# Performance work log

Measured on AMD Instinct MI355X. Metric: run time of the kernel, lower is better.

## Reference

```python
import jax, jax.numpy as jnp
import numpy as np
import math

V, E, L, MLP_RATIO = 16384, 768, 5, 4
B, S = 4, 1024
EPS = 1e-5


def setup_inputs() -> dict:
    key = jax.random.key(0)
    ks = jax.random.split(key, 20)
    sd = 0.02
    H = E * MLP_RATIO
    inp = {}
    inp["seq"] = jax.random.randint(ks[0], (B, S), 0, V)
    inp["pad_mask"] = jnp.zeros((B, S), dtype=bool)
    inp["embed"] = jax.random.normal(ks[1], (V, E), jnp.float32) * sd
    inp["enc_qkv_w"] = jax.random.normal(ks[2], (L, 3, E, E), jnp.float32) * sd
    inp["enc_qkv_b"] = jnp.zeros((L, 3, E), jnp.float32)
    inp["enc_ln"] = jnp.stack([jnp.ones((L, 2, E)), jnp.zeros((L, 2, E))], axis=2)  # [L,2,2,E] (gamma,beta)
    inp["enc_mlp_w1"] = jax.random.normal(ks[3], (L, E, H), jnp.float32) * sd
    inp["enc_mlp_b1"] = jnp.zeros((L, H), jnp.float32)
    inp["enc_mlp_w2"] = jax.random.normal(ks[4], (L, H, E), jnp.float32) * sd
    inp["enc_mlp_b2"] = jnp.zeros((L, E), jnp.float32)
    inp["dec_qkv_w"] = jax.random.normal(ks[5], (L, 6, E, E), jnp.float32) * sd  # q,k,v,q2,k2,v2
    inp["dec_qkv_b"] = jnp.zeros((L, 6, E), jnp.float32)
    inp["dec_ln"] = jnp.stack([jnp.ones((L, 3, E)), jnp.zeros((L, 3, E))], axis=2)  # [L,3,2,E]
    inp["dec_mlp_w1"] = jax.random.normal(ks[6], (L, E, H), jnp.float32) * sd
    inp["dec_mlp_b1"] = jnp.zeros((L, H), jnp.float32)
    inp["dec_mlp_w2"] = jax.random.normal(ks[7], (L, H, E), jnp.float32) * sd
    inp["dec_mlp_b2"] = jnp.zeros((L, E), jnp.float32)
    inp["unembed"] = jax.random.normal(ks[8], (E, V), jnp.float32) * sd
    return inp


def _layernorm(x, g, b):
    mu = jnp.mean(x, axis=-1, keepdims=True)
    var = jnp.mean((x - mu) ** 2, axis=-1, keepdims=True)
    return (x - mu) * jax.lax.rsqrt(var + EPS) * g + b


def reference(seq, pad_mask, embed, enc_qkv_w, enc_qkv_b, enc_ln,
              enc_mlp_w1, enc_mlp_b1, enc_mlp_w2, enc_mlp_b2,
              dec_qkv_w, dec_qkv_b, dec_ln,
              dec_mlp_w1, dec_mlp_b1, dec_mlp_w2, dec_mlp_b2, unembed):
    Bv, Sv = seq.shape
    Ev = embed.shape[1]
    scalar = 1.0 / math.sqrt(Ev)

    # RoPE tables over full E (single-head, as in source)
    inv_freq = 1.0 / (10000.0 ** (jnp.arange(0, Ev, 2, dtype=jnp.float32) / Ev))
    pos = jnp.arange(Sv, dtype=jnp.float32)
    freqs = pos[:, None] * inv_freq[None, :]  # [S, E/2]
    cos, sin = jnp.cos(freqs), jnp.sin(freqs)

    def rope(x):  # x: [B,S,E]
        x1, x2 = x[..., 0::2], x[..., 1::2]
        return jnp.stack((x1 * cos - x2 * sin, x1 * sin + x2 * cos), axis=-1).reshape(x.shape)

    neg = jnp.finfo(embed.dtype).min
    pad = pad_mask[:, None, :]  # [B,1,S] mask keys
    causal = jnp.triu(jnp.ones((Sv, Sv), dtype=bool), k=1)[None]  # [1,S,S]

    def attend(q, k, v, mask):
        scores = jnp.einsum('bse,bte->bst', q, k) * scalar
        scores = jnp.where(mask, neg, scores)
        return jnp.einsum('bst,bte->bse', jax.nn.softmax(scores, axis=-1), v)

    embeds = embed[seq]  # [B,S,E]

    # ---- encoder ----
    x = embeds
    enc_outs = []
    for i in range(enc_qkv_w.shape[0]):
        q = rope(x @ enc_qkv_w[i, 0] + enc_qkv_b[i, 0])
        k = rope(x @ enc_qkv_w[i, 1] + enc_qkv_b[i, 1])
        v = x @ enc_qkv_w[i, 2] + enc_qkv_b[i, 2]
        h = attend(q, k, v, pad)
        x = _layernorm(x + h, enc_ln[i, 0, 0], enc_ln[i, 0, 1])
        mlp = jax.nn.relu(jax.nn.relu(x @ enc_mlp_w1[i] + enc_mlp_b1[i]) @ enc_mlp_w2[i] + enc_mlp_b2[i])
        x = _layernorm(x + mlp, enc_ln[i, 1, 0], enc_ln[i, 1, 1])
        enc_outs.append(x)

    # ---- decoder ----
    x = embeds
    self_mask = causal | pad  # [B,S,S]
    for i in range(dec_qkv_w.shape[0]):
        kv = enc_outs[i]
        q = rope(x @ dec_qkv_w[i, 0] + dec_qkv_b[i, 0])
        k = rope(x @ dec_qkv_w[i, 1] + dec_qkv_b[i, 1])
        v = x @ dec_qkv_w[i, 2] + dec_qkv_b[i, 2]
        h1 = attend(q, k, v, self_mask)
        x = _layernorm(x + h1, dec_ln[i, 0, 0], dec_ln[i, 0, 1])
        q2 = rope(x @ dec_qkv_w[i, 3] + dec_qkv_b[i, 3])
        k2 = rope(kv @ dec_qkv_w[i, 4] + dec_qkv_b[i, 4])
        v2 = kv @ dec_qkv_w[i, 5] + dec_qkv_b[i, 5]
        h2 = attend(q2, k2, v2, pad)
        x = _layernorm(x + h2, dec_ln[i, 1, 0], dec_ln[i, 1, 1])
        mlp = jax.nn.relu(jax.nn.relu(x @ dec_mlp_w1[i] + dec_mlp_b1[i]) @ dec_mlp_w2[i] + dec_mlp_b2[i])
        x = _layernorm(x + mlp, dec_ln[i, 2, 0], dec_ln[i, 2, 1])

    return x @ unembed  # [B,S,V] logits
```

## Files before the change

### kernel.cpp

```cpp
#include <hip/hip_runtime.h>
#include <math.h>
#include <stdint.h>

#define B_ 4
#define S_ 1024
#define E_ 768
#define H_ 3072
#define V_ 16384
#define L_ 5
#define T_TOK 4096

typedef unsigned short u16;
typedef short bf16x8 __attribute__((ext_vector_type(8)));
typedef float floatx4 __attribute__((ext_vector_type(4)));
typedef u16 u16x4 __attribute__((ext_vector_type(4)));

__device__ __forceinline__ u16 f2bf(float f) {
    union { float f; unsigned u; } x; x.f = f;
    unsigned r = (x.u + 0x7FFFu + ((x.u >> 16) & 1u)) >> 16;
    return (u16)r;
}
__device__ __forceinline__ float bf2f(u16 v) {
    union { unsigned u; float f; } x; x.u = ((unsigned)v) << 16;
    return x.f;
}

__device__ __forceinline__ void gload16(const void* g, void* l) {
    __builtin_amdgcn_global_load_lds(
        (const __attribute__((address_space(1))) unsigned int*)(uintptr_t)g,
        (__attribute__((address_space(3))) unsigned int*)(uintptr_t)l,
        16, 0, 0);
}

__device__ __forceinline__ void bar_sync() {
    asm volatile("s_waitcnt vmcnt(0)" ::: "memory");
    __builtin_amdgcn_s_barrier();
    asm volatile("" ::: "memory");
}

__device__ __forceinline__ float rope_rot(float v, long row, long col, int lane,
                                          const float2* __restrict__ tab) {
    float vp = __shfl_xor(v, 1, 64);
    int s = (int)(row & (S_ - 1));
    int ii = ((int)col >> 1) % 384;
    float2 f = tab[(long)s * 384 + ii];
    return (lane & 1) ? (vp * f.y + v * f.x) : (v * f.x - vp * f.y);
}

#define BK 32

template<int OBF, int RELU, int BIAS, int ROPE>
__global__ __launch_bounds__(256) void mgemm(
    const u16* __restrict__ A, const u16* __restrict__ B, void* __restrict__ Cv,
    const float* __restrict__ bias, const float2* __restrict__ tab,
    float alpha, int M, int N, int K,
    int lda, int ldb, int ldc,
    long sA, long sB, long sC)
{
    __shared__ u16 As[2][128 * BK];
    __shared__ u16 Bs[2][128 * BK];

    const int tid  = threadIdx.x;
    const int lane = tid & 63;
    const int wid  = tid >> 6;
    const int wr   = (wid >> 1) * 64;
    const int wc   = (wid & 1) * 64;
    const int lr   = lane & 15;
    const int kg   = lane >> 4;

    const long rowBase = (long)blockIdx.y * 128;
    const long colBase = (long)blockIdx.x * 128;

    const u16* Ab = A + (long)blockIdx.z * sA;
    const u16* Bb = B + (long)blockIdx.z * sB;

    const int c0 = tid, c1 = tid + 256;
    const int ar0 = c0 >> 2, ac0 = (c0 & 3) ^ ((ar0 >> 1) & 3);
    const int ar1 = c1 >> 2, ac1 = (c1 & 3) ^ ((ar1 >> 1) & 3);

    const u16* pa0 = Ab + (rowBase + ar0) * (long)lda + ac0 * 8;
    const u16* pa1 = Ab + (rowBase + ar1) * (long)lda + ac1 * 8;
    const u16* pb0 = Bb + (colBase + ar0) * (long)ldb + ac0 * 8;
    const u16* pb1 = Bb + (colBase + ar1) * (long)ldb + ac1 * 8;

    int aoff[4], boff[4];
    #pragma unroll
    for (int m = 0; m < 4; ++m) {
        int r = wr + m * 16 + lr;
        aoff[m] = r * 32 + ((kg ^ ((r >> 1) & 3)) << 3);
        int c = wc + m * 16 + lr;
        boff[m] = c * 32 + ((kg ^ ((c >> 1) & 3)) << 3);
    }

    floatx4 acc[4][4];
    #pragma unroll
    for (int m = 0; m < 4; ++m)
        #pragma unroll
        for (int n = 0; n < 4; ++n)
            acc[m][n] = (floatx4)0.f;

    auto stage = [&](int buf, int k0) {
        gload16(pa0 + k0, &As[buf][c0 * 8]);
        gload16(pa1 + k0, &As[buf][c1 * 8]);
        gload16(pb0 + k0, &Bs[buf][c0 * 8]);
        gload16(pb1 + k0, &Bs[buf][c1 * 8]);
    };

    const int NT = K / BK;
    stage(0, 0);
    bar_sync();

    for (int t = 0; t < NT; ++t) {
        const int cur = t & 1;
        if (t + 1 < NT) stage(cur ^ 1, (t + 1) * BK);

        bf16x8 af[4], bfr[4];
        #pragma unroll
        for (int m = 0; m < 4; ++m) af[m]  = *(const bf16x8*)(&As[cur][aoff[m]]);
        #pragma unroll
        for (int n = 0; n < 4; ++n) bfr[n] = *(const bf16x8*)(&Bs[cur][boff[n]]);
        #pragma unroll
        for (int m = 0; m < 4; ++m)
            #pragma unroll
            for (int n = 0; n < 4; ++n)
                acc[m][n] = __builtin_amdgcn_mfma_f32_16x16x32_bf16(
                                af[m], bfr[n], acc[m][n], 0, 0, 0);

        if (t + 1 < NT) bar_sync();
    }

    const long col0 = colBase + wc + lr;
    const long row0 = rowBase + wr + kg * 4;
    #pragma unroll
    for (int n = 0; n < 4; ++n) {
        long col = col0 + n * 16;
        float bvc = (BIAS == 1) ? bias[col] : 0.f;
        #pragma unroll
        for (int m = 0; m < 4; ++m)
            #pragma unroll
            for (int j = 0; j < 4; ++j) {
                long row = row0 + m * 16 + j;
                float v = acc[m][n][j] * alpha + bvc;
                if (BIAS == 2) v += bias[row];
                if (ROPE) v = rope_rot(v, row, col, lane, tab);
                if (RELU) v = fmaxf(v, 0.f);
                if (OBF) ((u16*)Cv + (long)blockIdx.z * sC)[row * (long)ldc + col] = f2bf(v);
                else     ((float*)Cv + (long)blockIdx.z * sC)[row * (long)ldc + col] = v;
            }
    }
}

template<int OBF, int RELU, int BIAS, int ROPE>
__global__ __launch_bounds__(256) void mgemm64(
    const u16* __restrict__ A, const u16* __restrict__ B, void* __restrict__ Cv,
    const float* __restrict__ bias, const float2* __restrict__ tab,
    float alpha, int M, int N, int K,
    int lda, int ldb, int ldc,
    long sA, long sB, long sC)
{
    __shared__ u16 As[2][64 * BK];
    __shared__ u16 Bs[2][128 * BK];

    const int tid  = threadIdx.x;
    const int lane = tid & 63;
    const int wid  = tid >> 6;
    const int lr   = lane & 15;
    const int kg   = lane >> 4;

    const long rowBase = (long)blockIdx.y * 64;
    const long colBase = (long)blockIdx.x * 128;

    const u16* Ab = A + (long)blockIdx.z * sA;
    const u16* Bb = B + (long)blockIdx.z * sB;

    const int ra = tid >> 2, cha = (tid & 3) ^ ((ra >> 1) & 3);
    const int c0 = tid, c1 = tid + 256;
    const int rb0 = c0 >> 2, chb0 = (c0 & 3) ^ ((rb0 >> 1) & 3);
    const int rb1 = c1 >> 2, chb1 = (c1 & 3) ^ ((rb1 >> 1) & 3);

    const u16* pa  = Ab + (rowBase + ra)  * (long)lda + cha  * 8;
    const u16* pb0 = Bb + (colBase + rb0) * (long)ldb + chb0 * 8;
    const u16* pb1 = Bb + (colBase + rb1) * (long)ldb + chb1 * 8;

    int aoff[4], boff[2];
    #pragma unroll
    for (int m = 0; m < 4; ++m) {
        int r = m * 16 + lr;
        aoff[m] = r * 32 + ((kg ^ ((r >> 1) & 3)) << 3);
    }
    #pragma unroll
    for (int n = 0; n < 2; ++n) {
        int c = wid * 32 + n * 16 + lr;
        boff[n] = c * 32 + ((kg ^ ((c >> 1) & 3)) << 3);
    }

    floatx4 acc[4][2];
    #pragma unroll
    for (int m = 0; m < 4; ++m)
        #pragma unroll
        for (int n = 0; n < 2; ++n)
            acc[m][n] = (floatx4)0.f;

    auto stage = [&](int buf, int k0) {
        gload16(pa  + k0, &As[buf][tid * 8]);
        gload16(pb0 + k0, &Bs[buf][c0 * 8]);
        gload16(pb1 + k0, &Bs[buf][c1 * 8]);
    };

    const int NT = K / BK;
    stage(0, 0);
    bar_sync();

    for (int t = 0; t < NT; ++t) {
        const int cur = t & 1;
        if (t + 1 < NT) stage(cur ^ 1, (t + 1) * BK);

        bf16x8 af[4], bfr[2];
        #pragma unroll
        for (int m = 0; m < 4; ++m) af[m]  = *(const bf16x8*)(&As[cur][aoff[m]]);
        #pragma unroll
        for (int n = 0; n < 2; ++n) bfr[n] = *(const bf16x8*)(&Bs[cur][boff[n]]);
        #pragma unroll
        for (int m = 0; m < 4; ++m)
            #pragma unroll
            for (int n = 0; n < 2; ++n)
                acc[m][n] = __builtin_amdgcn_mfma_f32_16x16x32_bf16(
                                af[m], bfr[n], acc[m][n], 0, 0, 0);

        if (t + 1 < NT) bar_sync();
    }

    const long col0 = colBase + wid * 32 + lr;
    const long row0 = rowBase + kg * 4;
    #pragma unroll
    for (int n = 0; n < 2; ++n) {
        long col = col0 + n * 16;
        float bvc = (BIAS == 1) ? bias[col] : 0.f;
        #pragma unroll
        for (int m = 0; m < 4; ++m)
            #pragma unroll
            for (int j = 0; j < 4; ++j) {
                long row = row0 + m * 16 + j;
                float v = acc[m][n][j] * alpha + bvc;
                if (BIAS == 2) v += bias[row];
                if (ROPE) v = rope_rot(v, row, col, lane, tab);
                if (RELU) v = fmaxf(v, 0.f);
                if (OBF) ((u16*)Cv + (long)blockIdx.z * sC)[row * (long)ldc + col] = f2bf(v);
                else     ((float*)Cv + (long)blockIdx.z * sC)[row * (long)ldc + col] = v;
            }
    }
}

template<int OBF, int RELU, int BIAS>
__global__ __launch_bounds__(512, 2) void mgemm8(
    const u16* __restrict__ A, const u16* __restrict__ B, void* __restrict__ Cv,
    const float* __restrict__ bias, float alpha, int M, int N, int K,
    int lda, int ldb, int ldc)
{
    __shared__ u16 As[3][256 * 32];
    __shared__ u16 Bs[3][256 * 32];

    const int tid  = threadIdx.x;
    const int lane = tid & 63;
    const int wid  = tid >> 6;
    const int wm   = wid >> 2;
    const int wn   = wid & 3;
    const int lr   = lane & 15;
    const int kg   = lane >> 4;

    const long rowBase = (long)blockIdx.y * 256;
    const long colBase = (long)blockIdx.x * 256;

    const int c0 = tid, c1 = tid + 512;
    const int r0 = c0 >> 2, ch0 = (c0 & 3) ^ ((r0 >> 1) & 3);
    const int r1 = c1 >> 2, ch1 = (c1 & 3) ^ ((r1 >> 1) & 3);

    const u16* pa0 = A + (rowBase + r0) * (long)lda + ch0 * 8;
    const u16* pa1 = A + (rowBase + r1) * (long)lda + ch1 * 8;
    const u16* pb0 = B + (colBase + r0) * (long)ldb + ch0 * 8;
    const u16* pb1 = B + (colBase + r1) * (long)ldb + ch1 * 8;

    int aoff[8], boff[4];
    #pragma unroll
    for (int mi = 0; mi < 8; ++mi) {
        int r = wm * 128 + mi * 16 + lr;
        aoff[mi] = r * 32 + ((kg ^ ((r >> 1) & 3)) << 3);
    }
    #pragma unroll
    for (int ni = 0; ni < 4; ++ni) {
        int c = wn * 64 + ni * 16 + lr;
        boff[ni] = c * 32 + ((kg ^ ((c >> 1) & 3)) << 3);
    }

    floatx4 acc[8][4];
    #pragma unroll
    for (int mi = 0; mi < 8; ++mi)
        #pragma unroll
        for (int ni = 0; ni < 4; ++ni)
            acc[mi][ni] = (floatx4)0.f;

    auto stageA = [&](int buf, int kt) {
        gload16(pa0 + (long)kt * 32, &As[buf][c0 * 8]);
        gload16(pa1 + (long)kt * 32, &As[buf][c1 * 8]);
    };
    auto stageB = [&](int buf, int kt) {
        gload16(pb0 + (long)kt * 32, &Bs[buf][c0 * 8]);
        gload16(pb1 + (long)kt * 32, &Bs[buf][c1 * 8]);
    };

    const int NT = K / 32;
    stageA(0, 0); stageB(0, 0);
    stageA(1, 1); stageB(1, 1);
    asm volatile("s_waitcnt vmcnt(4)" ::: "memory");
    __builtin_amdgcn_sched_barrier(0);
    __builtin_amdgcn_s_barrier();

    int b0 = 0, b1 = 1, b2 = 2;
    for (int t = 0; t < NT; ++t) {
        bf16x8 afr[4], bfr[4];
        if (t + 2 < NT) stageA(b2, t + 2);
        #pragma unroll
        for (int mi = 0; mi < 4; ++mi) afr[mi] = *(const bf16x8*)(&As[b0][aoff[mi]]);
        #pragma unroll
        for (int ni = 0; ni < 4; ++ni) bfr[ni] = *(const bf16x8*)(&Bs[b0][boff[ni]]);
        __builtin_amdgcn_s_barrier();
        asm volatile("s_waitcnt lgkmcnt(0)" ::: "memory");
        __builtin_amdgcn_sched_barrier(0);
        __builtin_amdgcn_s_setprio(1);
        #pragma unroll
        for (int mi = 0; mi < 4; ++mi)
            #pragma unroll
            for (int ni = 0; ni < 4; ++ni)
                acc[mi][ni] = __builtin_amdgcn_mfma_f32_16x16x32_bf16(
                                  afr[mi], bfr[ni], acc[mi][ni], 0, 0, 0);
        __builtin_amdgcn_s_setprio(0);
        __builtin_amdgcn_sched_barrier(0);
        __builtin_amdgcn_s_barrier();
        if (t + 2 < NT) stageB(b2, t + 2);
        #pragma unroll
        for (int mi = 0; mi < 4; ++mi) afr[mi] = *(const bf16x8*)(&As[b0][aoff[4 + mi]]);
        __builtin_amdgcn_s_barrier();
        asm volatile("s_waitcnt lgkmcnt(0)" ::: "memory");
        __builtin_amdgcn_sched_barrier(0);
        __builtin_amdgcn_s_setprio(1);
        #pragma unroll
        for (int mi = 0; mi < 4; ++mi)
            #pragma unroll
            for (int ni = 0; ni < 4; ++ni)
                acc[4 + mi][ni] = __builtin_amdgcn_mfma_f32_16x16x32_bf16(
                                      afr[mi], bfr[ni], acc[4 + mi][ni], 0, 0, 0);
        __builtin_amdgcn_s_setprio(0);
        __builtin_amdgcn_sched_barrier(0);
        if (t + 2 < NT) { asm volatile("s_waitcnt vmcnt(4)" ::: "memory"); }
        else            { asm volatile("s_waitcnt vmcnt(0)" ::: "memory"); }
        __builtin_amdgcn_sched_barrier(0);
        __builtin_amdgcn_s_barrier();
        int tb = b0; b0 = b1; b1 = b2; b2 = tb;
    }

    const long col0 = colBase + wn * 64 + lr;
    const long row0 = rowBase + wm * 128 + kg * 4;
    #pragma unroll
    for (int ni = 0; ni < 4; ++ni) {
        long col = col0 + ni * 16;
        float bv = BIAS ? bias[col] : 0.f;
        #pragma unroll
        for (int mi = 0; mi < 8; ++mi)
            #pragma unroll
            for (int j = 0; j < 4; ++j) {
                float v = acc[mi][ni][j] * alpha + bv;
                if (RELU) v = fmaxf(v, 0.f);
                if (OBF) ((u16*)Cv)[(row0 + mi * 16 + j) * (long)ldc + col] = f2bf(v);
                else     ((float*)Cv)[(row0 + mi * 16 + j) * (long)ldc + col] = v;
            }
    }
}

__global__ __launch_bounds__(256) void tcvt(
    const float* __restrict__ in, u16* __restrict__ out,
    int ldIn, int ldOut, long sIn, long sOut)
{
    __shared__ u16 t[32][33];
    const int tx = threadIdx.x & 31, ty = threadIdx.x >> 5;
    const long r0 = (long)blockIdx.y * 32, c0 = (long)blockIdx.x * 32;
    const float* ib = in + (long)blockIdx.z * sIn;
    u16* ob = out + (long)blockIdx.z * sOut;
    #pragma unroll
    for (int j = 0; j < 4; ++j) {
        int r = ty + j * 8;
        t[r][tx] = f2bf(ib[(r0 + r) * (long)ldIn + c0 + tx]);
    }
    __syncthreads();
    #pragma unroll
    for (int j = 0; j < 4; ++j) {
        int c = ty + j * 8;
        ob[(c0 + c) * (long)ldOut + r0 + tx] = t[tx][c];
    }
}

__global__ __launch_bounds__(256) void gather_kernel(
    const int* __restrict__ seq, const float* __restrict__ embed,
    float* __restrict__ f_emb, float* __restrict__ f_x, u16* __restrict__ xb)
{
    int t = blockIdx.x;
    int tok = seq[t];
    const float* src = embed + (long)tok * E_;
    long base = (long)t * E_;
    #pragma unroll
    for (int j = 0; j < 3; ++j) {
        int i = threadIdx.x + j * 256;
        float v = src[i];
        f_emb[base + i] = v;
        f_x[base + i] = v;
        xb[base + i] = f2bf(v);
    }
}

__global__ __launch_bounds__(256) void seed_kernel(
    const float4* __restrict__ src, float4* __restrict__ x,
    u16* __restrict__ xb, long n4)
{
    long i = (long)blockIdx.x * blockDim.x + threadIdx.x;
    long stride = (long)gridDim.x * blockDim.x;
    for (; i < n4; i += stride) {
        float4 v = src[i];
        x[i] = v;
        u16x4 b = { f2bf(v.x), f2bf(v.y), f2bf(v.z), f2bf(v.w) };
        *(u16x4*)(xb + i * 4) = b;
    }
}

__global__ __launch_bounds__(384) void rope_tab_kernel(float2* __restrict__ tab)
{
    int s = blockIdx.x;
    int i = threadIdx.x;
    float inv = expf(-(float)(2 * i) * (9.210340371976184f / (float)E_));
    float ang = (float)s * inv;
    float sn, cs;
    sincosf(ang, &sn, &cs);
    tab[(long)s * 384 + i] = make_float2(cs, sn);
}

__global__ __launch_bounds__(256) void softmax_kernel(
    u16* __restrict__ P, int causal)
{
    __shared__ float sred[4];
    int row = blockIdx.x;
    int s = row & (S_ - 1);
    u16* p = P + (long)row * S_;
    int tid = threadIdx.x;
    int lane = tid & 63, wid = tid >> 6;

    u16x4 raw = *(const u16x4*)(p + tid * 4);
    float v[4];
    float mx = -INFINITY;
    #pragma unroll
    for (int j = 0; j < 4; ++j) {
        int col = tid * 4 + j;
        float val = bf2f(raw[j]);
        if (causal && col > s) val = -INFINITY;
        v[j] = val;
        mx = fmaxf(mx, val);
    }
    #pragma unroll
    for (int off = 1; off < 64; off <<= 1)
        mx = fmaxf(mx, __shfl_xor(mx, off, 64));
    if (lane == 0) sred[wid] = mx;
    __syncthreads();
    mx = fmaxf(fmaxf(sred[0], sred[1]), fmaxf(sred[2], sred[3]));
    __syncthreads();

    float sum = 0.f;
    #pragma unroll
    for (int j = 0; j < 4; ++j) {
        v[j] = __expf(v[j] - mx);
        sum += v[j];
    }
    #pragma unroll
    for (int off = 1; off < 64; off <<= 1)
        sum += __shfl_xor(sum, off, 64);
    if (lane == 0) sred[wid] = sum;
    __syncthreads();
    sum = sred[0] + sred[1] + sred[2] + sred[3];

    float invs = 1.f / sum;
    u16x4 o;
    #pragma unroll
    for (int j = 0; j < 4; ++j) o[j] = f2bf(v[j] * invs);
    *(u16x4*)(p + tid * 4) = o;
}

__global__ __launch_bounds__(256) void add_ln_kernel(
    float* __restrict__ x, const float* __restrict__ h,
    const float* __restrict__ gb, u16* __restrict__ xb)
{
    int row = blockIdx.x * 4 + (threadIdx.x >> 6);
    int lane = threadIdx.x & 63;
    float4* xr = (float4*)(x + (long)row * E_);
    const float4* hr = (const float4*)(h + (long)row * E_);

    float4 v[3];
    float sum = 0.f, sq = 0.f;
    #pragma unroll
    for (int l = 0; l < 3; ++l) {
        int idx = l * 64 + lane;
        float4 a = xr[idx];
        float4 b = hr[idx];
        v[l].x = a.x + b.x; v[l].y = a.y + b.y;
        v[l].z = a.z + b.z; v[l].w = a.w + b.w;
        sum += v[l].x + v[l].y + v[l].z + v[l].w;
        sq  += v[l].x*v[l].x + v[l].y*v[l].y + v[l].z*v[l].z + v[l].w*v[l].w;
    }
    #pragma unroll
    for (int off = 1; off < 64; off <<= 1) {
        sum += __shfl_xor(sum, off, 64);
        sq  += __shfl_xor(sq,  off, 64);
    }

    float mu  = sum * (1.f / E_);
    float var = sq * (1.f / E_) - mu * mu;
    float inv = rsqrtf(var + 1e-5f);

    const float4* g4 = (const float4*)gb;
    const float4* b4 = (const float4*)(gb + E_);
    #pragma unroll
    for (int l = 0; l < 3; ++l) {
        int idx = l * 64 + lane;
        float4 g = g4[idx], bb = b4[idx];
        float4 o;
        o.x = (v[l].x - mu) * inv * g.x + bb.x;
        o.y = (v[l].y - mu) * inv * g.y + bb.y;
        o.z = (v[l].z - mu) * inv * g.z + bb.z;
        o.w = (v[l].w - mu) * inv * g.w + bb.w;
        xr[idx] = o;
        u16x4 ob = { f2bf(o.x), f2bf(o.y), f2bf(o.z), f2bf(o.w) };
        *(u16x4*)(xb + (long)row * E_ + idx * 4) = ob;
    }
}

extern "C" void kernel_launch(void* const* d_in, const int* in_sizes, int n_in,
                              void* d_out, int out_size, void* d_ws, size_t ws_size,
                              hipStream_t stream) {
    const int*   seq       = (const int*)d_in[0];
    const float* embed     = (const float*)d_in[2];
    const float* enc_qkv_w = (const float*)d_in[3];
    const float* enc_qkv_b = (const float*)d_in[4];
    const float* enc_ln    = (const float*)d_in[5];
    const float* enc_w1    = (const float*)d_in[6];
    const float* enc_b1    = (const float*)d_in[7];
    const float* enc_w2    = (const float*)d_in[8];
    const float* enc_b2    = (const float*)d_in[9];
    const float* dec_qkv_w = (const float*)d_in[10];
    const float* dec_qkv_b = (const float*)d_in[11];
    const float* dec_ln    = (const float*)d_in[12];
    const float* dec_w1    = (const float*)d_in[13];
    const float* dec_b1    = (const float*)d_in[14];
    const float* dec_w2    = (const float*)d_in[15];
    const float* dec_b2    = (const float*)d_in[16];
    const float* unembed   = (const float*)d_in[17];

    const long TE  = (long)T_TOK * E_;
    const long TH  = (long)T_TOK * H_;
    const long SE  = (long)S_ * E_;
    const long SS  = (long)S_ * S_;
    const long SS4 = (long)B_ * SS;
    const long EE  = (long)E_ * E_;
    const long EH  = (long)E_ * H_;
    const long VE  = (long)V_ * E_;
    const long TQK = (long)T_TOK * 1536;
    const long SQK = (long)S_ * 1536;
    const long TABF = (long)S_ * 384 * 2;

    float*  ws    = (float*)d_ws;
    float*  f_x   = ws;
    float*  f_emb = ws + TE;
    float*  f_h   = ws + 2 * TE;
    float2* f_tab = (float2*)(ws + 3 * TE);

    u16* u_xb  = (u16*)(ws + 3 * TE + TABF);
    u16* u_enc = u_xb + TE;
    u16* u_qk  = u_enc + 5 * TE;
    u16* u_vT  = u_qk + TQK;
    u16* u_hid = u_vT + TE;
    u16* u_P   = u_hid + TH;
    u16* u_w   = u_P + SS4;

    const long WTOT = 45 * EE + 20 * EH + VE;
    size_t need_persist = (size_t)((char*)(u_w + WTOT) - (char*)d_ws);
    bool persist = ws_size >= need_persist;

    u16* pw_eqkv = u_w;
    u16* pw_dqkv = pw_eqkv + 15 * EE;
    u16* pw_ew1  = pw_dqkv + 30 * EE;
    u16* pw_ew2  = pw_ew1 + 5 * EH;
    u16* pw_dw1  = pw_ew2 + 5 * EH;
    u16* pw_dw2  = pw_dw1 + 5 * EH;
    u16* pw_un   = pw_dw2 + 5 * EH;

    const float SCALE = 0.03608439182435161f;

    auto T = [&](const float* in, u16* out, int R, int C, int z) {
        dim3 g(C / 32, R / 32, z);
        tcvt<<<g, 256, 0, stream>>>(in, out, C, R, (long)R * C, (long)R * C);
    };
    auto WTz = [&](const float* w, int R, int C, int z, u16* pp) -> const u16* {
        if (persist) return pp;
        T(w, u_w, R, C, z);
        return u_w;
    };

    if (persist) {
        T(enc_qkv_w, pw_eqkv, E_, E_, 15);
        T(dec_qkv_w, pw_dqkv, E_, E_, 30);
        T(enc_w1, pw_ew1, E_, H_, L_);
        T(enc_w2, pw_ew2, H_, E_, L_);
        T(dec_w1, pw_dw1, E_, H_, L_);
        T(dec_w2, pw_dw2, H_, E_, L_);
        T(unembed, pw_un, E_, V_, 1);
    }

    rope_tab_kernel<<<S_, 384, 0, stream>>>(f_tab);
    gather_kernel<<<T_TOK, 256, 0, stream>>>(seq, embed, f_emb, f_x, u_xb);

    auto qk_rope = [&](const u16* X, const u16* W, const float* bias) {
        dim3 g(1536 / 128, T_TOK / 128, 1);
        mgemm<1,0,1,1><<<g,256,0,stream>>>(X, W, u_qk, bias, f_tab, 1.f,
            T_TOK, 1536, E_, E_, E_, 1536, 0, 0, 0);
    };
    auto proj_rope64 = [&](const u16* X, const u16* W, u16* dst, const float* bias) {
        dim3 g(768 / 128, T_TOK / 64, 1);
        mgemm64<1,0,1,1><<<g,256,0,stream>>>(X, W, dst, bias, f_tab, 1.f,
            T_TOK, 768, E_, E_, E_, 1536, 0, 0, 0);
    };
    auto vT_gemm = [&](const u16* Wv, const u16* X, const float* biasrow) {
        dim3 g(T_TOK / 128, 768 / 64, 1);
        mgemm64<1,0,2,0><<<g,256,0,stream>>>(Wv, X, u_vT, biasrow, nullptr, 1.f,
            768, T_TOK, E_, E_, E_, T_TOK, 0, 0, 0);
    };
    auto qkt = [&]() {
        dim3 g(S_ / 128, S_ / 128, B_);
        mgemm<1,0,0,0><<<g,256,0,stream>>>(u_qk, u_qk + 768, u_P, nullptr, nullptr,
            SCALE, S_, S_, E_, 1536, 1536, S_, SQK, SQK, SS);
    };
    auto pv = [&]() {
        dim3 g(E_ / 128, S_ / 64, B_);
        mgemm64<0,0,0,0><<<g,256,0,stream>>>(u_P, u_vT, f_h, nullptr, nullptr, 1.f,
            S_, E_, S_, S_, T_TOK, E_, SS, 1024, SE);
    };
    auto mlp1 = [&](const u16* W, const float* b1) {
        dim3 g(H_ / 128, T_TOK / 128, 1);
        mgemm<1,1,1,0><<<g,256,0,stream>>>(u_xb, W, u_hid, b1, nullptr, 1.f,
            T_TOK, H_, E_, E_, E_, H_, 0, 0, 0);
    };
    auto mlp2 = [&](const u16* W, const float* b2) {
        dim3 g(E_ / 128, T_TOK / 64, 1);
        mgemm64<0,1,1,0><<<g,256,0,stream>>>(u_hid, W, f_h, b2, nullptr, 1.f,
            T_TOK, E_, H_, H_, H_, E_, 0, 0, 0);
    };
    auto lnz = [&](const float* gb, u16* xbdst) {
        add_ln_kernel<<<T_TOK / 4, 256, 0, stream>>>(f_x, f_h, gb, xbdst);
    };
    auto sm = [&](int causal) {
        softmax_kernel<<<T_TOK, 256, 0, stream>>>(u_P, causal);
    };

    for (int i = 0; i < L_; ++i) {
        const u16* xsrc = (i == 0) ? u_xb : u_enc + (long)(i - 1) * TE;
        const float* bb = enc_qkv_b + (long)i * 3 * E_;
        qk_rope(xsrc, WTz(enc_qkv_w + (long)i * 3 * EE, E_, E_, 2,
                          pw_eqkv + (long)i * 3 * EE), bb);
        vT_gemm(WTz(enc_qkv_w + ((long)i * 3 + 2) * EE, E_, E_, 1,
                    pw_eqkv + ((long)i * 3 + 2) * EE), xsrc, bb + 2 * E_);
        qkt();
        sm(0);
        pv();
        lnz(enc_ln + (2L * i + 0) * 2 * E_, u_xb);
        mlp1(WTz(enc_w1 + (long)i * EH, E_, H_, 1, pw_ew1 + (long)i * EH),
             enc_b1 + (long)i * H_);
        mlp2(WTz(enc_w2 + (long)i * EH, H_, E_, 1, pw_ew2 + (long)i * EH),
             enc_b2 + (long)i * E_);
        lnz(enc_ln + (2L * i + 1) * 2 * E_, u_enc + (long)i * TE);
    }

    seed_kernel<<<1024, 256, 0, stream>>>((const float4*)f_emb, (float4*)f_x, u_xb, TE / 4);
    for (int i = 0; i < L_; ++i) {
        const u16* kv_bf = u_enc + (long)i * TE;
        const float* bb = dec_qkv_b + (long)i * 6 * E_;

        qk_rope(u_xb, WTz(dec_qkv_w + (long)i * 6 * EE, E_, E_, 2,
                          pw_dqkv + (long)i * 6 * EE), bb);
        vT_gemm(WTz(dec_qkv_w + ((long)i * 6 + 2) * EE, E_, E_, 1,
                    pw_dqkv + ((long)i * 6 + 2) * EE), u_xb, bb + 2 * E_);
        qkt();
        sm(1);
        pv();
        lnz(dec_ln + (3L * i + 0) * 2 * E_, u_xb);

        proj_rope64(u_xb, WTz(dec_qkv_w + ((long)i * 6 + 3) * EE, E_, E_, 1,
                              pw_dqkv + ((long)i * 6 + 3) * EE), u_qk, bb + 3 * E_);
        proj_rope64(kv_bf, WTz(dec_qkv_w + ((long)i * 6 + 4) * EE, E_, E_, 1,
                               pw_dqkv + ((long)i * 6 + 4) * EE), u_qk + 768, bb + 4 * E_);
        vT_gemm(WTz(dec_qkv_w + ((long)i * 6 + 5) * EE, E_, E_, 1,
                    pw_dqkv + ((long)i * 6 + 5) * EE), kv_bf, bb + 5 * E_);
        qkt();
        sm(0);
        pv();
        lnz(dec_ln + (3L * i + 1) * 2 * E_, u_xb);

        mlp1(WTz(dec_w1 + (long)i * EH, E_, H_, 1, pw_dw1 + (long)i * EH),
             dec_b1 + (long)i * H_);
        mlp2(WTz(dec_w2 + (long)i * EH, H_, E_, 1, pw_dw2 + (long)i * EH),
             dec_b2 + (long)i * E_);
        lnz(dec_ln + (3L * i + 2) * 2 * E_, u_xb);
    }

    {
        dim3 g(V_ / 256, T_TOK / 256, 1);
        mgemm8<0,0,0><<<g,512,0,stream>>>(u_xb, WTz(unembed, E_, V_, 1, pw_un),
            d_out, nullptr, 1.f, T_TOK, V_, E_, E_, E_, V_);
    }
}
```

Measured before the change: 2.616 ms.

## Keep residual stream and sublayer outputs in bf16 instead of fp32

```diff
diff --git a/kernel.cpp b/kernel.cpp
--- a/kernel.cpp
+++ b/kernel.cpp
@@ -400,7 +400,7 @@
 
 __global__ __launch_bounds__(256) void gather_kernel(
     const int* __restrict__ seq, const float* __restrict__ embed,
-    float* __restrict__ f_emb, float* __restrict__ f_x, u16* __restrict__ xb)
+    u16* __restrict__ xb)
 {
     int t = blockIdx.x;
     int tok = seq[t];
@@ -409,25 +409,15 @@
     #pragma unroll
     for (int j = 0; j < 3; ++j) {
         int i = threadIdx.x + j * 256;
-        float v = src[i];
-        f_emb[base + i] = v;
-        f_x[base + i] = v;
-        xb[base + i] = f2bf(v);
-    }
-}
-
-__global__ __launch_bounds__(256) void seed_kernel(
-    const float4* __restrict__ src, float4* __restrict__ x,
-    u16* __restrict__ xb, long n4)
+        xb[base + i] = f2bf(src[i]);
+    }
+}
+
+__global__ __launch_bounds__(256) void copy_kernel(
+    const float4* __restrict__ src, float4* __restrict__ dst, long n)
 {
     long i = (long)blockIdx.x * blockDim.x + threadIdx.x;
-    long stride = (long)gridDim.x * blockDim.x;
-    for (; i < n4; i += stride) {
-        float4 v = src[i];
-        x[i] = v;
-        u16x4 b = { f2bf(v.x), f2bf(v.y), f2bf(v.z), f2bf(v.w) };
-        *(u16x4*)(xb + i * 4) = b;
-    }
+    if (i < n) dst[i] = src[i];
 }
 
 __global__ __launch_bounds__(384) void rope_tab_kernel(float2* __restrict__ tab)
@@ -491,23 +481,25 @@
 }
 
 __global__ __launch_bounds__(256) void add_ln_kernel(
-    float* __restrict__ x, const float* __restrict__ h,
-    const float* __restrict__ gb, u16* __restrict__ xb)
+    const u16* __restrict__ xin, const u16* __restrict__ hin,
+    const float* __restrict__ gb, u16* __restrict__ xout)
 {
     int row = blockIdx.x * 4 + (threadIdx.x >> 6);
     int lane = threadIdx.x & 63;
-    float4* xr = (float4*)(x + (long)row * E_);
-    const float4* hr = (const float4*)(h + (long)row * E_);
+    const u16x4* xr = (const u16x4*)(xin + (long)row * E_);
+    const u16x4* hr = (const u16x4*)(hin + (long)row * E_);
 
     float4 v[3];
     float sum = 0.f, sq = 0.f;
     #pragma unroll
     for (int l = 0; l < 3; ++l) {
         int idx = l * 64 + lane;
-        float4 a = xr[idx];
-        float4 b = hr[idx];
-        v[l].x = a.x + b.x; v[l].y = a.y + b.y;
-        v[l].z = a.z + b.z; v[l].w = a.w + b.w;
+        u16x4 a = xr[idx];
+        u16x4 b = hr[idx];
+        v[l].x = bf2f(a[0]) + bf2f(b[0]);
+        v[l].y = bf2f(a[1]) + bf2f(b[1]);
+        v[l].z = bf2f(a[2]) + bf2f(b[2]);
+        v[l].w = bf2f(a[3]) + bf2f(b[3]);
         sum += v[l].x + v[l].y + v[l].z + v[l].w;
         sq  += v[l].x*v[l].x + v[l].y*v[l].y + v[l].z*v[l].z + v[l].w*v[l].w;
     }
@@ -523,18 +515,17 @@
 
     const float4* g4 = (const float4*)gb;
     const float4* b4 = (const float4*)(gb + E_);
+    u16x4* xo = (u16x4*)(xout + (long)row * E_);
     #pragma unroll
     for (int l = 0; l < 3; ++l) {
         int idx = l * 64 + lane;
         float4 g = g4[idx], bb = b4[idx];
-        float4 o;
-        o.x = (v[l].x - mu) * inv * g.x + bb.x;
-        o.y = (v[l].y - mu) * inv * g.y + bb.y;
-        o.z = (v[l].z - mu) * inv * g.z + bb.z;
-        o.w = (v[l].w - mu) * inv * g.w + bb.w;
-        xr[idx] = o;
-        u16x4 ob = { f2bf(o.x), f2bf(o.y), f2bf(o.z), f2bf(o.w) };
-        *(u16x4*)(xb + (long)row * E_ + idx * 4) = ob;
+        u16x4 ob;
+        ob[0] = f2bf((v[l].x - mu) * inv * g.x + bb.x);
+        ob[1] = f2bf((v[l].y - mu) * inv * g.y + bb.y);
+        ob[2] = f2bf((v[l].z - mu) * inv * g.z + bb.z);
+        ob[3] = f2bf((v[l].w - mu) * inv * g.w + bb.w);
+        xo[idx] = ob;
     }
 }
 
@@ -572,13 +563,12 @@
     const long TABF = (long)S_ * 384 * 2;
 
     float*  ws    = (float*)d_ws;
-    float*  f_x   = ws;
-    float*  f_emb = ws + TE;
-    float*  f_h   = ws + 2 * TE;
-    float2* f_tab = (float2*)(ws + 3 * TE);
-
-    u16* u_xb  = (u16*)(ws + 3 * TE + TABF);
-    u16* u_enc = u_xb + TE;
+    float2* f_tab = (float2*)ws;
+
+    u16* u_emb = (u16*)(ws + TABF);
+    u16* u_x   = u_emb + TE;
+    u16* u_h   = u_x + TE;
+    u16* u_enc = u_h + TE;
     u16* u_qk  = u_enc + 5 * TE;
     u16* u_vT  = u_qk + TQK;
     u16* u_hid = u_vT + TE;
@@ -620,7 +610,7 @@
     }
 
     rope_tab_kernel<<<S_, 384, 0, stream>>>(f_tab);
-    gather_kernel<<<T_TOK, 256, 0, stream>>>(seq, embed, f_emb, f_x, u_xb);
+    gather_kernel<<<T_TOK, 256, 0, stream>>>(seq, embed, u_emb);
 
     auto qk_rope = [&](const u16* X, const u16* W, const float* bias) {
         dim3 g(1536 / 128, T_TOK / 128, 1);
@@ -644,28 +634,28 @@
     };
     auto pv = [&]() {
         dim3 g(E_ / 128, S_ / 64, B_);
-        mgemm64<0,0,0,0><<<g,256,0,stream>>>(u_P, u_vT, f_h, nullptr, nullptr, 1.f,
+        mgemm64<1,0,0,0><<<g,256,0,stream>>>(u_P, u_vT, u_h, nullptr, nullptr, 1.f,
             S_, E_, S_, S_, T_TOK, E_, SS, 1024, SE);
     };
-    auto mlp1 = [&](const u16* W, const float* b1) {
+    auto mlp1 = [&](const u16* X, const u16* W, const float* b1) {
         dim3 g(H_ / 128, T_TOK / 128, 1);
-        mgemm<1,1,1,0><<<g,256,0,stream>>>(u_xb, W, u_hid, b1, nullptr, 1.f,
+        mgemm<1,1,1,0><<<g,256,0,stream>>>(X, W, u_hid, b1, nullptr, 1.f,
             T_TOK, H_, E_, E_, E_, H_, 0, 0, 0);
     };
     auto mlp2 = [&](const u16* W, const float* b2) {
         dim3 g(E_ / 128, T_TOK / 64, 1);
-        mgemm64<0,1,1,0><<<g,256,0,stream>>>(u_hid, W, f_h, b2, nullptr, 1.f,
+        mgemm64<1,1,1,0><<<g,256,0,stream>>>(u_hid, W, u_h, b2, nullptr, 1.f,
             T_TOK, E_, H_, H_, H_, E_, 0, 0, 0);
     };
-    auto lnz = [&](const float* gb, u16* xbdst) {
-        add_ln_kernel<<<T_TOK / 4, 256, 0, stream>>>(f_x, f_h, gb, xbdst);
+    auto lnz = [&](const u16* xin, const float* gb, u16* xbdst) {
+        add_ln_kernel<<<T_TOK / 4, 256, 0, stream>>>(xin, u_h, gb, xbdst);
     };
     auto sm = [&](int causal) {
         softmax_kernel<<<T_TOK, 256, 0, stream>>>(u_P, causal);
     };
 
     for (int i = 0; i < L_; ++i) {
-        const u16* xsrc = (i == 0) ? u_xb : u_enc + (long)(i - 1) * TE;
+        const u16* xsrc = (i == 0) ? u_emb : u_enc + (long)(i - 1) * TE;
         const float* bb = enc_qkv_b + (long)i * 3 * E_;
         qk_rope(xsrc, WTz(enc_qkv_w + (long)i * 3 * EE, E_, E_, 2,
                           pw_eqkv + (long)i * 3 * EE), bb);
@@ -674,30 +664,31 @@
         qkt();
         sm(0);
         pv();
-        lnz(enc_ln + (2L * i + 0) * 2 * E_, u_xb);
-        mlp1(WTz(enc_w1 + (long)i * EH, E_, H_, 1, pw_ew1 + (long)i * EH),
+        lnz(xsrc, enc_ln + (2L * i + 0) * 2 * E_, u_x);
+        mlp1(u_x, WTz(enc_w1 + (long)i * EH, E_, H_, 1, pw_ew1 + (long)i * EH),
              enc_b1 + (long)i * H_);
         mlp2(WTz(enc_w2 + (long)i * EH, H_, E_, 1, pw_ew2 + (long)i * EH),
              enc_b2 + (long)i * E_);
-        lnz(enc_ln + (2L * i + 1) * 2 * E_, u_enc + (long)i * TE);
-    }
-
-    seed_kernel<<<1024, 256, 0, stream>>>((const float4*)f_emb, (float4*)f_x, u_xb, TE / 4);
+        lnz(u_x, enc_ln + (2L * i + 1) * 2 * E_, u_enc + (long)i * TE);
+    }
+
+    copy_kernel<<<(TE / 8 + 255) / 256, 256, 0, stream>>>(
+        (const float4*)u_emb, (float4*)u_x, TE / 8);
     for (int i = 0; i < L_; ++i) {
         const u16* kv_bf = u_enc + (long)i * TE;
         const float* bb = dec_qkv_b + (long)i * 6 * E_;
 
-        qk_rope(u_xb, WTz(dec_qkv_w + (long)i * 6 * EE, E_, E_, 2,
-                          pw_dqkv + (long)i * 6 * EE), bb);
+        qk_rope(u_x, WTz(dec_qkv_w + (long)i * 6 * EE, E_, E_, 2,
+                         pw_dqkv + (long)i * 6 * EE), bb);
         vT_gemm(WTz(dec_qkv_w + ((long)i * 6 + 2) * EE, E_, E_, 1,
-                    pw_dqkv + ((long)i * 6 + 2) * EE), u_xb, bb + 2 * E_);
+                    pw_dqkv + ((long)i * 6 + 2) * EE), u_x, bb + 2 * E_);
         qkt();
         sm(1);
         pv();
-        lnz(dec_ln + (3L * i + 0) * 2 * E_, u_xb);
-
-        proj_rope64(u_xb, WTz(dec_qkv_w + ((long)i * 6 + 3) * EE, E_, E_, 1,
-                              pw_dqkv + ((long)i * 6 + 3) * EE), u_qk, bb + 3 * E_);
+        lnz(u_x, dec_ln + (3L * i + 0) * 2 * E_, u_x);
+
+        proj_rope64(u_x, WTz(dec_qkv_w + ((long)i * 6 + 3) * EE, E_, E_, 1,
+                             pw_dqkv + ((long)i * 6 + 3) * EE), u_qk, bb + 3 * E_);
         proj_rope64(kv_bf, WTz(dec_qkv_w + ((long)i * 6 + 4) * EE, E_, E_, 1,
                                pw_dqkv + ((long)i * 6 + 4) * EE), u_qk + 768, bb + 4 * E_);
         vT_gemm(WTz(dec_qkv_w + ((long)i * 6 + 5) * EE, E_, E_, 1,
@@ -705,18 +696,18 @@
         qkt();
         sm(0);
         pv();
-        lnz(dec_ln + (3L * i + 1) * 2 * E_, u_xb);
-
-        mlp1(WTz(dec_w1 + (long)i * EH, E_, H_, 1, pw_dw1 + (long)i * EH),
+        lnz(u_x, dec_ln + (3L * i + 1) * 2 * E_, u_x);
+
+        mlp1(u_x, WTz(dec_w1 + (long)i * EH, E_, H_, 1, pw_dw1 + (long)i * EH),
              dec_b1 + (long)i * H_);
         mlp2(WTz(dec_w2 + (long)i * EH, H_, E_, 1, pw_dw2 + (long)i * EH),
              dec_b2 + (long)i * E_);
-        lnz(dec_ln + (3L * i + 2) * 2 * E_, u_xb);
+        lnz(u_x, dec_ln + (3L * i + 2) * 2 * E_, u_x);
     }
 
     {
         dim3 g(V_ / 256, T_TOK / 256, 1);
-        mgemm8<0,0,0><<<g,512,0,stream>>>(u_xb, WTz(unembed, E_, V_, 1, pw_un),
+        mgemm8<0,0,0><<<g,512,0,stream>>>(u_x, WTz(unembed, E_, V_, 1, pw_un),
             d_out, nullptr, 1.f, T_TOK, V_, E_, E_, E_, V_);
     }
 }
```

New measurement: 2.519 ms. 1.04x faster.
